# Optimization experiments

Measured on AMD Instinct MI355X. Metric: run time of the kernel, lower is better.

Reference implementation:

```python
import jax, jax.numpy as jnp
import numpy as np
import math

B, L, HID = 2, 2048, 1024
NH, DH = 16, 64
MASK_VAL = -1000000000.0  # half_precision_flag == False


def setup_inputs() -> dict:
    key = jax.random.key(0)
    ks = jax.random.split(key, 12)
    s = 0.02
    return {
        "queries": jax.random.normal(ks[0], (B, L, HID), jnp.float32),
        "keys": jax.random.normal(ks[1], (B, L, HID), jnp.float32),
        "values": jax.random.normal(ks[2], (B, L, HID), jnp.float32),
        "mask": jax.random.randint(ks[3], (B, L, L), 0, 2, jnp.int32),
        "Wq": jax.random.normal(ks[4], (HID, NH * DH), jnp.float32) * s,
        "bq": jnp.zeros((NH * DH,), jnp.float32),
        "Wk": jax.random.normal(ks[5], (HID, NH * DH), jnp.float32) * s,
        "bk": jnp.zeros((NH * DH,), jnp.float32),
        "Wv": jax.random.normal(ks[6], (HID, NH * DH), jnp.float32) * s,
        "bv": jnp.zeros((NH * DH,), jnp.float32),
        "Wo": jax.random.normal(ks[7], (NH * DH, HID), jnp.float32) * s,
        "bo": jnp.zeros((HID,), jnp.float32),
    }


def reference(queries, keys, values, mask, Wq, bq, Wk, bk, Wv, bv, Wo, bo):
    # Linear projections: (B, L, NH*DH)
    q = queries @ Wq + bq
    k = keys @ Wk + bk
    v = values @ Wv + bv
    # FAITHFUL to original: raw .view(B, NH, -1, DH) without transpose
    q = q.reshape(B, NH, L, DH)
    k = k.reshape(B, NH, L, DH)
    v = v.reshape(B, NH, L, DH)
    # scaled dot-product scores: (B, NH, L, L)
    scores = jnp.einsum("bhqd,bhkd->bhqk", q, k) / math.sqrt(DH)
    scores = jnp.where(mask[:, None, :, :] == 0, MASK_VAL, scores)
    probs = jax.nn.softmax(scores, axis=-1)  # dropout p=0 -> identity
    ctx = jnp.einsum("bhqk,bhkd->bhqd", probs, v)  # (B, NH, L, DH)
    # transpose(1,2) then flatten heads, as in original
    ctx = ctx.transpose(0, 2, 1, 3).reshape(B, L, NH * DH)
    return ctx @ Wo + bo
```

## Files before the change

kernel.cpp:

```cpp
#include <hip/hip_runtime.h>
#include <stdint.h>

typedef __bf16 bf16;
typedef __bf16 bf16x8 __attribute__((ext_vector_type(8)));
typedef __bf16 bf16x4 __attribute__((ext_vector_type(4)));
typedef float  f32x4  __attribute__((ext_vector_type(4)));
typedef short  s16x4  __attribute__((ext_vector_type(4)));
typedef unsigned long long ull;

#define GLOAD16(gptr, lptr)                                                     \
  __builtin_amdgcn_global_load_lds(                                             \
      (const __attribute__((address_space(1))) void*)(gptr),                    \
      (__attribute__((address_space(3))) void*)(lptr), 16, 0, 0)

#define MFMA16(a, b, c) __builtin_amdgcn_mfma_f32_16x16x32_bf16((a), (b), (c), 0, 0, 0)
#define MFMA16K16(a, b, c) __builtin_amdgcn_mfma_f32_16x16x16bf16_1k((a), (b), (c), 0, 0, 0)

static constexpr int B_ = 2, L_ = 2048, NH_ = 16, DH_ = 64;
static constexpr float QSCALE = 0.18033688011112042f;

__global__ void k_cvt3(const float* __restrict__ q, const float* __restrict__ k,
                       const float* __restrict__ v, bf16* __restrict__ outbase) {
  const float* in = blockIdx.y == 0 ? q : (blockIdx.y == 1 ? k : v);
  bf16* out = outbase + (size_t)blockIdx.y * 4194304;
  int i = blockIdx.x * blockDim.x + threadIdx.x;
  const float4 f = ((const float4*)in)[i];
  bf16x4 o = {(bf16)f.x, (bf16)f.y, (bf16)f.z, (bf16)f.w};
  ((bf16x4*)out)[i] = o;
}

__global__ void k_wtrans4(const float* __restrict__ wq, const float* __restrict__ wk,
                          const float* __restrict__ wv, const float* __restrict__ wo,
                          bf16* __restrict__ outbase) {
  const int z = blockIdx.z;
  const float* in = z == 0 ? wq : (z == 1 ? wk : (z == 2 ? wv : wo));
  bf16* out = outbase + (size_t)z * 1048576;
  __shared__ float t[32][33];
  int bx = blockIdx.x * 32, by = blockIdx.y * 32;
  int x = threadIdx.x & 31, y = threadIdx.x >> 5;
#pragma unroll
  for (int r = 0; r < 4; ++r)
    t[y + r * 8][x] = in[(size_t)(by + y + r * 8) * 1024 + bx + x];
  __syncthreads();
#pragma unroll
  for (int r = 0; r < 4; ++r)
    out[(size_t)(bx + y + r * 8) * 1024 + by + x] = (bf16)t[x][y + r * 8];
}

__global__ void k_maskbits(const int* __restrict__ mask, ull* __restrict__ mb) {
  int t = blockIdx.x * blockDim.x + threadIdx.x;
  ull bal = __ballot(mask[t] != 0);
  if ((threadIdx.x & 63) == 0) mb[t >> 6] = bal;
}

__global__ __launch_bounds__(256) void k_gemm3(const bf16* __restrict__ Xb,
                                               const bf16* __restrict__ Wb,
                                               const float* __restrict__ b0,
                                               const float* __restrict__ b1,
                                               const float* __restrict__ b2,
                                               bf16* __restrict__ Ob) {
  const int z = blockIdx.z;
  const bf16* A  = Xb + (size_t)z * 4194304;
  const bf16* Bt = Wb + (size_t)z * 1048576;
  const float* bias = z == 0 ? b0 : (z == 1 ? b1 : b2);
  bf16* C = Ob + (size_t)z * 4194304;
  const int m0 = blockIdx.y * 128, n0 = blockIdx.x * 128;
  __shared__ __align__(16) bf16 As[128 * 32];
  __shared__ __align__(16) bf16 Bs[128 * 32];
  const int tid = threadIdx.x, lane = tid & 63, w = tid >> 6, quad = lane >> 4, l15 = lane & 15;
  const int wm = (w & 1) * 64, wn = (w >> 1) * 64;
  f32x4 acc[4][4] = {};
  for (int kt = 0; kt < 32; ++kt) {
    const int kk = kt * 32;
#pragma unroll
    for (int i = 0; i < 2; ++i) {
      int s = tid + i * 256;
      int r = s >> 2, c = (s & 3) ^ ((r >> 1) & 3);
      GLOAD16(A + (size_t)(m0 + r) * 1024 + kk + c * 8, As + s * 8);
      GLOAD16(Bt + (size_t)(n0 + r) * 1024 + kk + c * 8, Bs + s * 8);
    }
    __syncthreads();
    bf16x8 af[4], bb[4];
#pragma unroll
    for (int i = 0; i < 4; ++i) {
      int ra = wm + i * 16 + l15, rb = wn + i * 16 + l15;
      af[i] = *(const bf16x8*)(As + (ra * 4 + (quad ^ ((ra >> 1) & 3))) * 8);
      bb[i] = *(const bf16x8*)(Bs + (rb * 4 + (quad ^ ((rb >> 1) & 3))) * 8);
    }
#pragma unroll
    for (int mi = 0; mi < 4; ++mi)
#pragma unroll
      for (int ni = 0; ni < 4; ++ni)
        acc[mi][ni] = MFMA16(af[mi], bb[ni], acc[mi][ni]);
    __syncthreads();
  }
  const float scale = (z == 0) ? QSCALE : 1.0f;
#pragma unroll
  for (int mi = 0; mi < 4; ++mi)
#pragma unroll
    for (int ni = 0; ni < 4; ++ni) {
      int row = m0 + wm + mi * 16 + quad * 4;
      int col = n0 + wn + ni * 16 + l15;
      float bz = bias[col];
      if (z == 2) {
        int b_ = row >> 11, l = row & 2047;
        int hh = l >> 7;
        int i0 = (l & 127) * 16 + (col >> 6);
        int d  = col & 63;
        bf16* dst = C + (size_t)(b_ * 16 + hh) * 131072;
#pragma unroll
        for (int r = 0; r < 4; ++r) {
          int iK = i0 + 16 * r;
          dst[((size_t)(iK >> 2) * 64 + d) * 4 + (iK & 3)] = (bf16)(acc[mi][ni][r] + bz);
        }
      } else {
#pragma unroll
        for (int r = 0; r < 4; ++r)
          C[(size_t)(row + r) * 1024 + col] = (bf16)((acc[mi][ni][r] + bz) * scale);
      }
    }
}

__global__ __launch_bounds__(256) void k_gemmo(const bf16* __restrict__ A,
                                               const bf16* __restrict__ Bt,
                                               const float* __restrict__ bias,
                                               float* __restrict__ C) {
  const int m0 = blockIdx.y * 64, n0 = blockIdx.x * 128;
  __shared__ __align__(16) bf16 As[64 * 32];
  __shared__ __align__(16) bf16 Bs[128 * 32];
  const int tid = threadIdx.x, lane = tid & 63, w = tid >> 6, quad = lane >> 4, l15 = lane & 15;
  const int wn = w * 32;
  f32x4 acc[4][2] = {};
  for (int kt = 0; kt < 32; ++kt) {
    const int kk = kt * 32;
    {
      int r = tid >> 2, c = (tid & 3) ^ ((r >> 1) & 3);
      GLOAD16(A + (size_t)(m0 + r) * 1024 + kk + c * 8, As + tid * 8);
    }
#pragma unroll
    for (int i = 0; i < 2; ++i) {
      int s = tid + i * 256;
      int r = s >> 2, c = (s & 3) ^ ((r >> 1) & 3);
      GLOAD16(Bt + (size_t)(n0 + r) * 1024 + kk + c * 8, Bs + s * 8);
    }
    __syncthreads();
    bf16x8 af[4], bb[2];
#pragma unroll
    for (int i = 0; i < 4; ++i) {
      int ra = i * 16 + l15;
      af[i] = *(const bf16x8*)(As + (ra * 4 + (quad ^ ((ra >> 1) & 3))) * 8);
    }
#pragma unroll
    for (int i = 0; i < 2; ++i) {
      int rb = wn + i * 16 + l15;
      bb[i] = *(const bf16x8*)(Bs + (rb * 4 + (quad ^ ((rb >> 1) & 3))) * 8);
    }
#pragma unroll
    for (int mi = 0; mi < 4; ++mi)
#pragma unroll
      for (int ni = 0; ni < 2; ++ni)
        acc[mi][ni] = MFMA16(af[mi], bb[ni], acc[mi][ni]);
    __syncthreads();
  }
#pragma unroll
  for (int mi = 0; mi < 4; ++mi)
#pragma unroll
    for (int ni = 0; ni < 2; ++ni) {
      int row = m0 + mi * 16 + quad * 4;
      int col = n0 + wn + ni * 16 + l15;
      float bz = bias[col];
#pragma unroll
      for (int r = 0; r < 4; ++r)
        C[(size_t)(row + r) * 1024 + col] = acc[mi][ni][r] + bz;
    }
}

__global__ __launch_bounds__(256) void k_flash(const bf16* __restrict__ Qp,
                                               const bf16* __restrict__ Kp,
                                               const bf16* __restrict__ Vtp,
                                               const ull* __restrict__ mb,
                                               bf16* __restrict__ ctx) {
  const int b = blockIdx.z, h = blockIdx.y, q0 = blockIdx.x * 128;
  const size_t HEAD = 131072;
  const bf16* Q  = Qp  + ((size_t)b * NH_ + h) * HEAD;
  const bf16* K  = Kp  + ((size_t)b * NH_ + h) * HEAD;
  const bf16* Vt = Vtp + ((size_t)b * NH_ + h) * HEAD;
  const ull* mrow = mb + (size_t)b * L_ * 32;

  __shared__ __align__(16) bf16 Ks[2][64 * 64];
  __shared__ __align__(16) bf16 Vs[2][64 * 64];
  __shared__ __align__(16) ull  Ms[2][256];

  const int tid = threadIdx.x, lane = tid & 63, w = tid >> 6, quad = lane >> 4, l15 = lane & 15;

  bf16x8 qf[2][2];
#pragma unroll
  for (int qb = 0; qb < 2; ++qb)
#pragma unroll
    for (int ks = 0; ks < 2; ++ks)
      qf[qb][ks] = *(const bf16x8*)(Q + (size_t)(q0 + w * 32 + qb * 16 + l15) * 64 + ks * 32 + quad * 8);

#pragma unroll
  for (int i = 0; i < 2; ++i) {
    int s = tid + i * 256;
    int key = s >> 3, c = (s & 7) ^ (key & 7);
    GLOAD16(K + (size_t)key * 64 + c * 8, Ks[0] + s * 8);
    GLOAD16(Vt + (size_t)s * 8, Vs[0] + s * 8);
  }
  if (w < 2) {
    int r = w * 64 + lane;
    GLOAD16(mrow + (size_t)(q0 + r) * 32, (bf16*)&Ms[0][0] + r * 8);
  }
  __syncthreads();

  f32x4 accO[2][4] = {};
  float lsum[2] = {0.f, 0.f};

  for (int kt = 0; kt < 32; ++kt) {
    const int cur = kt & 1;
    if (kt + 1 < 32) {
      const int nxt = cur ^ 1;
#pragma unroll
      for (int i = 0; i < 2; ++i) {
        int s = tid + i * 256;
        int key = s >> 3, c = (s & 7) ^ (key & 7);
        GLOAD16(K + (size_t)((kt + 1) * 64 + key) * 64 + c * 8, Ks[nxt] + s * 8);
        GLOAD16(Vt + (size_t)(kt + 1) * 4096 + s * 8, Vs[nxt] + s * 8);
      }
      if ((kt & 1) && w < 2) {
        int r = w * 64 + lane;
        GLOAD16(mrow + (size_t)(q0 + r) * 32 + (kt + 1),
                (bf16*)&Ms[((kt + 1) >> 1) & 1][0] + r * 8);
      }
    }

    f32x4 st[4][2] = {};
#pragma unroll
    for (int ks = 0; ks < 2; ++ks)
#pragma unroll
      for (int kb = 0; kb < 4; ++kb) {
        int key = kb * 16 + l15;
        bf16x8 kf = *(const bf16x8*)(Ks[cur] + (key * 8 + ((ks * 4 + quad) ^ (key & 7))) * 8);
        st[kb][0] = MFMA16(kf, qf[0][ks], st[kb][0]);
        st[kb][1] = MFMA16(kf, qf[1][ks], st[kb][1]);
      }

    const ull* Mcur = Ms[(kt >> 1) & 1];
    const ull word0 = Mcur[(w * 32 + l15) * 2 + cur];
    const ull word1 = Mcur[(w * 32 + 16 + l15) * 2 + cur];
    s16x4 pf[4][2];
#pragma unroll
    for (int kb = 0; kb < 4; ++kb)
#pragma unroll
      for (int qb = 0; qb < 2; ++qb) {
        const unsigned nib = (unsigned)((qb ? word1 : word0) >> (kb * 16 + quad * 4)) & 0xFu;
        float p0 = (nib & 1u) ? __builtin_amdgcn_exp2f(st[kb][qb][0]) : 0.f;
        float p1 = (nib & 2u) ? __builtin_amdgcn_exp2f(st[kb][qb][1]) : 0.f;
        float p2 = (nib & 4u) ? __builtin_amdgcn_exp2f(st[kb][qb][2]) : 0.f;
        float p3 = (nib & 8u) ? __builtin_amdgcn_exp2f(st[kb][qb][3]) : 0.f;
        lsum[qb] += (p0 + p1) + (p2 + p3);
        bf16x4 pb = {(bf16)p0, (bf16)p1, (bf16)p2, (bf16)p3};
        pf[kb][qb] = __builtin_bit_cast(s16x4, pb);
      }

#pragma unroll
    for (int kb = 0; kb < 4; ++kb)
#pragma unroll
      for (int db = 0; db < 4; ++db) {
        s16x4 vf = *(const s16x4*)(Vs[cur] + ((size_t)((kb * 4 + quad) * 64 + db * 16 + l15)) * 4);
        accO[0][db] = MFMA16K16(pf[kb][0], vf, accO[0][db]);
        accO[1][db] = MFMA16K16(pf[kb][1], vf, accO[1][db]);
      }
    __syncthreads();
  }

#pragma unroll
  for (int qb = 0; qb < 2; ++qb) {
    lsum[qb] += __shfl_xor(lsum[qb], 16, 64);
    lsum[qb] += __shfl_xor(lsum[qb], 32, 64);
  }
#pragma unroll
  for (int qb = 0; qb < 2; ++qb) {
    float rl[4];
#pragma unroll
    for (int r = 0; r < 4; ++r)
      rl[r] = 1.0f / __shfl(lsum[qb], quad * 4 + r, 64);
#pragma unroll
    for (int db = 0; db < 4; ++db) {
      const int col = h * 64 + db * 16 + l15;
#pragma unroll
      for (int r = 0; r < 4; ++r) {
        const int rowg = q0 + w * 32 + qb * 16 + quad * 4 + r;
        ctx[((size_t)b * L_ + rowg) * 1024 + col] = (bf16)(accO[qb][db][r] * rl[r]);
      }
    }
  }
}

extern "C" void kernel_launch(void* const* d_in, const int* in_sizes, int n_in,
                              void* d_out, int out_size, void* d_ws, size_t ws_size,
                              hipStream_t stream) {
  (void)in_sizes; (void)n_in; (void)out_size; (void)ws_size;
  const float* q    = (const float*)d_in[0];
  const float* k    = (const float*)d_in[1];
  const float* v    = (const float*)d_in[2];
  const int*   mask = (const int*)d_in[3];
  const float* Wq = (const float*)d_in[4];
  const float* bq = (const float*)d_in[5];
  const float* Wk = (const float*)d_in[6];
  const float* bk = (const float*)d_in[7];
  const float* Wv = (const float*)d_in[8];
  const float* bv = (const float*)d_in[9];
  const float* Wo = (const float*)d_in[10];
  const float* bo = (const float*)d_in[11];
  float* out = (float*)d_out;

  char* ws = (char*)d_ws;
  const size_t SX = (size_t)4096 * 1024 * 2;
  const size_t SW = (size_t)1024 * 1024 * 2;
  bf16* X   = (bf16*)(ws);
  bf16* Wt  = (bf16*)(ws + 3 * SX);
  bf16* QKV = (bf16*)(ws + 3 * SX + 4 * SW);
  bf16* Qp  = QKV;
  bf16* Kp  = QKV + 4194304;
  bf16* Vtp = QKV + 2 * 4194304;
  bf16* Ctx = (bf16*)(ws + 6 * SX + 4 * SW);
  ull* mbits = (ull*)(ws + 7 * SX + 4 * SW);

  dim3 blk(256);
  k_cvt3<<<dim3(4096, 3), blk, 0, stream>>>(q, k, v, X);
  k_wtrans4<<<dim3(32, 32, 4), blk, 0, stream>>>(Wq, Wk, Wv, Wo, Wt);
  k_maskbits<<<32768, blk, 0, stream>>>(mask, mbits);

  k_gemm3<<<dim3(8, 32, 3), blk, 0, stream>>>(X, Wt, bq, bk, bv, QKV);

  k_flash<<<dim3(16, NH_, B_), blk, 0, stream>>>(Qp, Kp, Vtp, mbits, Ctx);

  k_gemmo<<<dim3(8, 64), blk, 0, stream>>>(Ctx, Wt + 3 * 1048576, bo, out);
}
```

Measured before the change: 280.4 us.

## Halve flash query tile, compute row sums via MFMA, deepen gemm3 K-tile

The flash kernel now handles 64 query rows per block instead of 128, doubling the grid to 1024 blocks so more work is spread across CUs. The per-row softmax denominator is now accumulated with an extra MFMA against a ones vector instead of scalar adds plus cross-lane shuffles. Separately, the QKV GEMM uses a 64-wide K tile with an 8-way XOR swizzle, halving its loop iterations and barriers. The tradeoff is that each K/V tile loaded into shared memory is reused by half as many query rows, which doubles K/V global traffic.

```diff
diff --git a/kernel.cpp b/kernel.cpp
--- a/kernel.cpp
+++ b/kernel.cpp
@@ -65,33 +65,36 @@
   const float* bias = z == 0 ? b0 : (z == 1 ? b1 : b2);
   bf16* C = Ob + (size_t)z * 4194304;
   const int m0 = blockIdx.y * 128, n0 = blockIdx.x * 128;
-  __shared__ __align__(16) bf16 As[128 * 32];
-  __shared__ __align__(16) bf16 Bs[128 * 32];
+  __shared__ __align__(16) bf16 As[128 * 64];
+  __shared__ __align__(16) bf16 Bs[128 * 64];
   const int tid = threadIdx.x, lane = tid & 63, w = tid >> 6, quad = lane >> 4, l15 = lane & 15;
   const int wm = (w & 1) * 64, wn = (w >> 1) * 64;
   f32x4 acc[4][4] = {};
-  for (int kt = 0; kt < 32; ++kt) {
-    const int kk = kt * 32;
-#pragma unroll
-    for (int i = 0; i < 2; ++i) {
+  for (int kt = 0; kt < 16; ++kt) {
+    const int kk = kt * 64;
+#pragma unroll
+    for (int i = 0; i < 4; ++i) {
       int s = tid + i * 256;
-      int r = s >> 2, c = (s & 3) ^ ((r >> 1) & 3);
+      int r = s >> 3, c = (s & 7) ^ (r & 7);
       GLOAD16(A + (size_t)(m0 + r) * 1024 + kk + c * 8, As + s * 8);
       GLOAD16(Bt + (size_t)(n0 + r) * 1024 + kk + c * 8, Bs + s * 8);
     }
     __syncthreads();
-    bf16x8 af[4], bb[4];
-#pragma unroll
-    for (int i = 0; i < 4; ++i) {
-      int ra = wm + i * 16 + l15, rb = wn + i * 16 + l15;
-      af[i] = *(const bf16x8*)(As + (ra * 4 + (quad ^ ((ra >> 1) & 3))) * 8);
-      bb[i] = *(const bf16x8*)(Bs + (rb * 4 + (quad ^ ((rb >> 1) & 3))) * 8);
-    }
-#pragma unroll
-    for (int mi = 0; mi < 4; ++mi)
-#pragma unroll
-      for (int ni = 0; ni < 4; ++ni)
-        acc[mi][ni] = MFMA16(af[mi], bb[ni], acc[mi][ni]);
+#pragma unroll
+    for (int ks = 0; ks < 2; ++ks) {
+      bf16x8 af[4], bb[4];
+#pragma unroll
+      for (int i = 0; i < 4; ++i) {
+        int ra = wm + i * 16 + l15, rb = wn + i * 16 + l15;
+        af[i] = *(const bf16x8*)(As + (ra * 8 + ((ks * 4 + quad) ^ (ra & 7))) * 8);
+        bb[i] = *(const bf16x8*)(Bs + (rb * 8 + ((ks * 4 + quad) ^ (rb & 7))) * 8);
+      }
+#pragma unroll
+      for (int mi = 0; mi < 4; ++mi)
+#pragma unroll
+        for (int ni = 0; ni < 4; ++ni)
+          acc[mi][ni] = MFMA16(af[mi], bb[ni], acc[mi][ni]);
+    }
     __syncthreads();
   }
   const float scale = (z == 0) ? QSCALE : 1.0f;
@@ -180,7 +183,7 @@
                                                const bf16* __restrict__ Vtp,
                                                const ull* __restrict__ mb,
                                                bf16* __restrict__ ctx) {
-  const int b = blockIdx.z, h = blockIdx.y, q0 = blockIdx.x * 128;
+  const int b = blockIdx.z, h = blockIdx.y, q0 = blockIdx.x * 64;
   const size_t HEAD = 131072;
   const bf16* Q  = Qp  + ((size_t)b * NH_ + h) * HEAD;
   const bf16* K  = Kp  + ((size_t)b * NH_ + h) * HEAD;
@@ -189,16 +192,14 @@
 
   __shared__ __align__(16) bf16 Ks[2][64 * 64];
   __shared__ __align__(16) bf16 Vs[2][64 * 64];
-  __shared__ __align__(16) ull  Ms[2][256];
+  __shared__ __align__(16) ull  Ms[2][128];
 
   const int tid = threadIdx.x, lane = tid & 63, w = tid >> 6, quad = lane >> 4, l15 = lane & 15;
 
-  bf16x8 qf[2][2];
-#pragma unroll
-  for (int qb = 0; qb < 2; ++qb)
-#pragma unroll
-    for (int ks = 0; ks < 2; ++ks)
-      qf[qb][ks] = *(const bf16x8*)(Q + (size_t)(q0 + w * 32 + qb * 16 + l15) * 64 + ks * 32 + quad * 8);
+  bf16x8 qf[2];
+#pragma unroll
+  for (int ks = 0; ks < 2; ++ks)
+    qf[ks] = *(const bf16x8*)(Q + (size_t)(q0 + w * 16 + l15) * 64 + ks * 32 + quad * 8);
 
 #pragma unroll
   for (int i = 0; i < 2; ++i) {
@@ -207,14 +208,12 @@
     GLOAD16(K + (size_t)key * 64 + c * 8, Ks[0] + s * 8);
     GLOAD16(Vt + (size_t)s * 8, Vs[0] + s * 8);
   }
-  if (w < 2) {
-    int r = w * 64 + lane;
-    GLOAD16(mrow + (size_t)(q0 + r) * 32, (bf16*)&Ms[0][0] + r * 8);
-  }
+  if (w == 0) GLOAD16(mrow + (size_t)(q0 + lane) * 32, (bf16*)&Ms[0][0] + lane * 8);
   __syncthreads();
 
-  f32x4 accO[2][4] = {};
-  float lsum[2] = {0.f, 0.f};
+  f32x4 accO[4] = {};
+  f32x4 accL = {};
+  const s16x4 onesf = {0x3F80, 0x3F80, 0x3F80, 0x3F80};
 
   for (int kt = 0; kt < 32; ++kt) {
     const int cur = kt & 1;
@@ -227,72 +226,58 @@
         GLOAD16(K + (size_t)((kt + 1) * 64 + key) * 64 + c * 8, Ks[nxt] + s * 8);
         GLOAD16(Vt + (size_t)(kt + 1) * 4096 + s * 8, Vs[nxt] + s * 8);
       }
-      if ((kt & 1) && w < 2) {
-        int r = w * 64 + lane;
-        GLOAD16(mrow + (size_t)(q0 + r) * 32 + (kt + 1),
-                (bf16*)&Ms[((kt + 1) >> 1) & 1][0] + r * 8);
-      }
-    }
-
-    f32x4 st[4][2] = {};
+      if ((kt & 1) && w == 0)
+        GLOAD16(mrow + (size_t)(q0 + lane) * 32 + (kt + 1),
+                (bf16*)&Ms[((kt + 1) >> 1) & 1][0] + lane * 8);
+    }
+
+    f32x4 st[4] = {};
 #pragma unroll
     for (int ks = 0; ks < 2; ++ks)
 #pragma unroll
       for (int kb = 0; kb < 4; ++kb) {
         int key = kb * 16 + l15;
         bf16x8 kf = *(const bf16x8*)(Ks[cur] + (key * 8 + ((ks * 4 + quad) ^ (key & 7))) * 8);
-        st[kb][0] = MFMA16(kf, qf[0][ks], st[kb][0]);
-        st[kb][1] = MFMA16(kf, qf[1][ks], st[kb][1]);
-      }
-
-    const ull* Mcur = Ms[(kt >> 1) & 1];
-    const ull word0 = Mcur[(w * 32 + l15) * 2 + cur];
-    const ull word1 = Mcur[(w * 32 + 16 + l15) * 2 + cur];
-    s16x4 pf[4][2];
+        st[kb] = MFMA16(kf, qf[ks], st[kb]);
+      }
+
+    const ull word = Ms[(kt >> 1) & 1][(w * 16 + l15) * 2 + cur];
+    s16x4 pf[4];
+#pragma unroll
+    for (int kb = 0; kb < 4; ++kb) {
+      const unsigned nib = (unsigned)(word >> (kb * 16 + quad * 4)) & 0xFu;
+      float p0 = (nib & 1u) ? __builtin_amdgcn_exp2f(st[kb][0]) : 0.f;
+      float p1 = (nib & 2u) ? __builtin_amdgcn_exp2f(st[kb][1]) : 0.f;
+      float p2 = (nib & 4u) ? __builtin_amdgcn_exp2f(st[kb][2]) : 0.f;
+      float p3 = (nib & 8u) ? __builtin_amdgcn_exp2f(st[kb][3]) : 0.f;
+      bf16x4 pb = {(bf16)p0, (bf16)p1, (bf16)p2, (bf16)p3};
+      pf[kb] = __builtin_bit_cast(s16x4, pb);
+    }
+
 #pragma unroll
     for (int kb = 0; kb < 4; ++kb)
-#pragma unroll
-      for (int qb = 0; qb < 2; ++qb) {
-        const unsigned nib = (unsigned)((qb ? word1 : word0) >> (kb * 16 + quad * 4)) & 0xFu;
-        float p0 = (nib & 1u) ? __builtin_amdgcn_exp2f(st[kb][qb][0]) : 0.f;
-        float p1 = (nib & 2u) ? __builtin_amdgcn_exp2f(st[kb][qb][1]) : 0.f;
-        float p2 = (nib & 4u) ? __builtin_amdgcn_exp2f(st[kb][qb][2]) : 0.f;
-        float p3 = (nib & 8u) ? __builtin_amdgcn_exp2f(st[kb][qb][3]) : 0.f;
-        lsum[qb] += (p0 + p1) + (p2 + p3);
-        bf16x4 pb = {(bf16)p0, (bf16)p1, (bf16)p2, (bf16)p3};
-        pf[kb][qb] = __builtin_bit_cast(s16x4, pb);
-      }
+      accL = MFMA16K16(pf[kb], onesf, accL);
 
 #pragma unroll
     for (int kb = 0; kb < 4; ++kb)
 #pragma unroll
       for (int db = 0; db < 4; ++db) {
         s16x4 vf = *(const s16x4*)(Vs[cur] + ((size_t)((kb * 4 + quad) * 64 + db * 16 + l15)) * 4);
-        accO[0][db] = MFMA16K16(pf[kb][0], vf, accO[0][db]);
-        accO[1][db] = MFMA16K16(pf[kb][1], vf, accO[1][db]);
-      }
-    __syncthreads();
-  }
-
-#pragma unroll
-  for (int qb = 0; qb < 2; ++qb) {
-    lsum[qb] += __shfl_xor(lsum[qb], 16, 64);
-    lsum[qb] += __shfl_xor(lsum[qb], 32, 64);
-  }
-#pragma unroll
-  for (int qb = 0; qb < 2; ++qb) {
-    float rl[4];
-#pragma unroll
-    for (int r = 0; r < 4; ++r)
-      rl[r] = 1.0f / __shfl(lsum[qb], quad * 4 + r, 64);
-#pragma unroll
-    for (int db = 0; db < 4; ++db) {
-      const int col = h * 64 + db * 16 + l15;
-#pragma unroll
-      for (int r = 0; r < 4; ++r) {
-        const int rowg = q0 + w * 32 + qb * 16 + quad * 4 + r;
-        ctx[((size_t)b * L_ + rowg) * 1024 + col] = (bf16)(accO[qb][db][r] * rl[r]);
-      }
+        accO[db] = MFMA16K16(pf[kb], vf, accO[db]);
+      }
+    __syncthreads();
+  }
+
+  float rl[4];
+#pragma unroll
+  for (int r = 0; r < 4; ++r) rl[r] = 1.0f / accL[r];
+#pragma unroll
+  for (int db = 0; db < 4; ++db) {
+    const int col = h * 64 + db * 16 + l15;
+#pragma unroll
+    for (int r = 0; r < 4; ++r) {
+      const int rowg = q0 + w * 16 + quad * 4 + r;
+      ctx[((size_t)b * L_ + rowg) * 1024 + col] = (bf16)(accO[db][r] * rl[r]);
     }
   }
 }
@@ -334,7 +319,7 @@
 
   k_gemm3<<<dim3(8, 32, 3), blk, 0, stream>>>(X, Wt, bq, bk, bv, QKV);
 
-  k_flash<<<dim3(16, NH_, B_), blk, 0, stream>>>(Qp, Kp, Vtp, mbits, Ctx);
+  k_flash<<<dim3(32, NH_, B_), blk, 0, stream>>>(Qp, Kp, Vtp, mbits, Ctx);
 
   k_gemmo<<<dim3(8, 64), blk, 0, stream>>>(Ctx, Wt + 3 * 1048576, bo, out);
 }
```

After: 291.0 us. 3.8% more time.
